# Optimization experiments

Measured on AMD Instinct MI355X. Metric: run time of the kernel, lower is better.

The kernel has to match this reference:

```python
import jax, jax.numpy as jnp
import numpy as np

ALPHAS = (0.1, 0.3, 0.6)
WEIGHTS = (0.5, 0.3, 0.2)
HUBER_MARGIN = 1.0
B, S = 2048, 8192


def setup_inputs() -> dict:
    key = jax.random.key(0)
    k1, k2 = jax.random.split(key)
    pred = jax.random.normal(k1, (B, S), dtype=jnp.float32)
    target = jax.random.normal(k2, (B, S), dtype=jnp.float32)
    return {"pred": pred, "target": target}


def _ema(x, alpha):
    # x: [B, S]; ema[0] = x[0]; ema[i] = alpha*x[i] + (1-alpha)*ema[i-1]
    x0 = x[:, 0]
    def step(carry, xi):
        nc = alpha * xi + (1.0 - alpha) * carry
        return nc, nc
    _, ys = jax.lax.scan(step, x0, x[:, 1:].T)  # ys: [S-1, B]
    return jnp.concatenate([x0[:, None], ys.T], axis=1)  # [B, S]


def _huber_loss(pred_delta, target_delta):
    dir_agreement = pred_delta * target_delta
    step_err = jnp.abs(pred_delta - target_delta)
    quad = jnp.square(jnp.maximum(HUBER_MARGIN - dir_agreement, 0.0)) / (2.0 * HUBER_MARGIN)
    return jnp.where(dir_agreement < 0, step_err, quad).mean(axis=1)  # [B]


def reference(pred, target):
    loss = jnp.zeros((pred.shape[0],), dtype=pred.dtype)
    for alpha, weight in zip(ALPHAS, WEIGHTS):
        pe = _ema(pred, alpha)
        te = _ema(target, alpha)
        pd = pe[:, 1:] - pe[:, :-1]
        td = te[:, 1:] - te[:, :-1]
        loss = loss + weight * _huber_loss(pd, td)
    return loss.mean()  # reduction='mean'
```

## Files before the change

### kernel.cpp

```cpp
#include <hip/hip_runtime.h>

#define B_ROWS 2048
#define S_LEN  8192
#define PER_LANE 16
#define TPB 512
#define WPB 8
#define CHUNK (64 * PER_LANE)
#define NBLOCKS B_ROWS

constexpr double cpowi(double b, int e) { double r = 1.0; for (int i = 0; i < e; ++i) r *= b; return r; }
constexpr float tof(double x) { return (x < 1.2e-38 && x > -1.2e-38) ? 0.0f : (float)x; }

#define W0f 0.9f
#define W1f 0.7f
#define W2f 0.4f
#define SE0 0.2f
#define SE1 0.6f
#define SE2 1.2f
constexpr float NA0 = -(0.1f * 0.1f);
constexpr float NA1 = -(0.3f * 0.3f);
constexpr float NA2 = -(0.6f * 0.6f);

constexpr float D0_1 = tof(cpowi(0.9, 16)),  D0_2 = tof(cpowi(0.9, 32));
constexpr float D0_4 = tof(cpowi(0.9, 64)),  D0_8 = tof(cpowi(0.9, 128));
constexpr float D1_1 = tof(cpowi(0.7, 16)),  D1_2 = tof(cpowi(0.7, 32));
constexpr float D2_1 = tof(cpowi(0.4, 16));

#define L2_0 (-0.15200309344504997f)
#define L2_1 (-0.51457317282975830f)
#define L2_2 (-1.32192809488736230f)

__device__ __forceinline__ float scan4(float v, int lane, float d1, float d2, float d4, float d8) {
    float u;
    u = __shfl_up(v, 1); v += (lane >= 1 ? d1 : 0.0f) * u;
    u = __shfl_up(v, 2); v += (lane >= 2 ? d2 : 0.0f) * u;
    u = __shfl_up(v, 4); v += (lane >= 4 ? d4 : 0.0f) * u;
    u = __shfl_up(v, 8); v += (lane >= 8 ? d8 : 0.0f) * u;
    return v;
}
__device__ __forceinline__ float scan2(float v, int lane, float d1, float d2) {
    float u;
    u = __shfl_up(v, 1); v += (lane >= 1 ? d1 : 0.0f) * u;
    u = __shfl_up(v, 2); v += (lane >= 2 ? d2 : 0.0f) * u;
    return v;
}
__device__ __forceinline__ float scan1(float v, int lane, float d1) {
    float u;
    u = __shfl_up(v, 1); v += (lane >= 1 ? d1 : 0.0f) * u;
    return v;
}

__global__ void __launch_bounds__(TPB, 4) msl_main(const float* __restrict__ pred,
                                                   const float* __restrict__ targ,
                                                   float* __restrict__ partial) {
    const int lane = threadIdx.x & 63;
    const int wave = threadIdx.x >> 6;
    const float* __restrict__ prow = pred + (size_t)blockIdx.x * S_LEN;
    const float* __restrict__ trow = targ + (size_t)blockIdx.x * S_LEN;
    const int base = wave * CHUNK + lane * PER_LANE;

    __shared__ float dxs[WPB][2][PER_LANE][64];
    __shared__ float sex[WPB][6];
    __shared__ float sred[WPB];

    const bool w0 = (wave == 0);
    const bool lz = (lane == 0);

    float pv0p = 0.f, pv0t = 0.f;
    if (lz && wave > 0) { pv0p = prow[base - 1]; pv0t = trow[base - 1]; }

    float xp[PER_LANE], xt[PER_LANE];
    {
        const float4* p4 = reinterpret_cast<const float4*>(prow + base);
        const float4* t4 = reinterpret_cast<const float4*>(trow + base);
#pragma unroll
        for (int j = 0; j < PER_LANE / 4; ++j) {
            float4 a = p4[j];
            float4 b = t4[j];
            xp[4 * j + 0] = a.x; xp[4 * j + 1] = a.y; xp[4 * j + 2] = a.z; xp[4 * j + 3] = a.w;
            xt[4 * j + 0] = b.x; xt[4 * j + 1] = b.y; xt[4 * j + 2] = b.z; xt[4 * j + 3] = b.w;
        }
    }

    float pvp = __shfl_up(xp[PER_LANE - 1], 1);
    float pvt = __shfl_up(xt[PER_LANE - 1], 1);
    if (lz) {
        pvp = w0 ? xp[0] : pv0p;
        pvt = w0 ? xt[0] : pv0t;
    }

    float Mp0 = 0.f, Mp1 = 0.f, Mp2 = 0.f, Mt0 = 0.f, Mt1 = 0.f, Mt2 = 0.f;
    float prevp = pvp, prevt = pvt;
#pragma unroll
    for (int j = 0; j < PER_LANE; ++j) {
        float dxp = xp[j] - prevp; prevp = xp[j];
        float dxt = xt[j] - prevt; prevt = xt[j];
        dxs[wave][0][j][lane] = dxp;
        dxs[wave][1][j][lane] = dxt;
        Mp0 = fmaf(W0f, Mp0, dxp);
        Mp1 = fmaf(W1f, Mp1, dxp);
        Mp2 = fmaf(W2f, Mp2, dxp);
        Mt0 = fmaf(W0f, Mt0, dxt);
        Mt1 = fmaf(W1f, Mt1, dxt);
        Mt2 = fmaf(W2f, Mt2, dxt);
    }

    float vp0 = scan4(Mp0, lane, D0_1, D0_2, D0_4, D0_8);
    float vp1 = scan2(Mp1, lane, D1_1, D1_2);
    float vp2 = scan1(Mp2, lane, D2_1);
    float vt0 = scan4(Mt0, lane, D0_1, D0_2, D0_4, D0_8);
    float vt1 = scan2(Mt1, lane, D1_1, D1_2);
    float vt2 = scan1(Mt2, lane, D2_1);

    if (lane == 63) {
        sex[wave][0] = vp0; sex[wave][1] = vp1; sex[wave][2] = vp2;
        sex[wave][3] = vt0; sex[wave][4] = vt1; sex[wave][5] = vt2;
    }
    __syncthreads();

    float Cp0 = 0.f, Cp1 = 0.f, Cp2 = 0.f, Ct0 = 0.f, Ct1 = 0.f, Ct2 = 0.f;
    if (wave > 0) {
        Cp0 = sex[wave - 1][0]; Cp1 = sex[wave - 1][1]; Cp2 = sex[wave - 1][2];
        Ct0 = sex[wave - 1][3]; Ct1 = sex[wave - 1][4]; Ct2 = sex[wave - 1][5];
    }

    const float e  = (float)(PER_LANE * lane);
    const float G0 = exp2f(e * L2_0);
    const float G1 = exp2f(e * L2_1);
    const float G2 = exp2f(e * L2_2);

    float up0 = __shfl_up(vp0, 1), up1 = __shfl_up(vp1, 1), up2 = __shfl_up(vp2, 1);
    float ut0 = __shfl_up(vt0, 1), ut1 = __shfl_up(vt1, 1), ut2 = __shfl_up(vt2, 1);

    float yp0 = lz ? (w0 ? 0.0f : Cp0) : fmaf(G0, Cp0, up0);
    float yp1 = lz ? (w0 ? 0.0f : Cp1) : fmaf(G1, Cp1, up1);
    float yp2 = lz ? (w0 ? 0.0f : Cp2) : fmaf(G2, Cp2, up2);
    float yt0 = lz ? (w0 ? 0.0f : Ct0) : fmaf(G0, Ct0, ut0);
    float yt1 = lz ? (w0 ? 0.0f : Ct1) : fmaf(G1, Ct1, ut1);
    float yt2 = lz ? (w0 ? 0.0f : Ct2) : fmaf(G2, Ct2, ut2);

    float acc0 = 0.f, acc1 = 0.f, acc2 = 0.f;
    const float skip = (w0 && lz) ? 0.0f : 1.0f;
#pragma unroll
    for (int j = 0; j < PER_LANE; ++j) {
        float dxp = dxs[wave][0][j][lane];
        float dxt = dxs[wave][1][j][lane];
        yp0 = fmaf(W0f, yp0, dxp);
        yt0 = fmaf(W0f, yt0, dxt);
        yp1 = fmaf(W1f, yp1, dxp);
        yt1 = fmaf(W1f, yt1, dxt);
        yp2 = fmaf(W2f, yp2, dxp);
        yt2 = fmaf(W2f, yt2, dxt);

        float m0 = yp0 * yt0, m1 = yp1 * yt1, m2 = yp2 * yt2;
        float se0 = SE0 * fabsf(yp0 - yt0);
        float se1 = SE1 * fabsf(yp1 - yt1);
        float se2 = SE2 * fabsf(yp2 - yt2);
        float mm0 = fmaxf(fmaf(NA0, m0, 1.0f), 0.0f);
        float mm1 = fmaxf(fmaf(NA1, m1, 1.0f), 0.0f);
        float mm2 = fmaxf(fmaf(NA2, m2, 1.0f), 0.0f);
        float h0 = (m0 < 0.0f) ? se0 : mm0 * mm0;
        float h1 = (m1 < 0.0f) ? se1 : mm1 * mm1;
        float h2 = (m2 < 0.0f) ? se2 : mm2 * mm2;
        if (j == 0) { h0 *= skip; h1 *= skip; h2 *= skip; }
        acc0 += h0; acc1 += h1; acc2 += h2;
    }

    float wacc = 0.25f * acc0 + 0.15f * acc1 + 0.10f * acc2;
#pragma unroll
    for (int o = 32; o > 0; o >>= 1) wacc += __shfl_down(wacc, o);

    if (lz) sred[wave] = wacc;
    __syncthreads();
    if (threadIdx.x == 0) {
        float s = 0.f;
#pragma unroll
        for (int i = 0; i < WPB; ++i) s += sred[i];
        partial[blockIdx.x] = s;
    }
}

__global__ void __launch_bounds__(256) msl_reduce(const float* __restrict__ partial,
                                                  float* __restrict__ out) {
    const int tid = threadIdx.x;
    float v = 0.f;
#pragma unroll
    for (int k = 0; k < NBLOCKS / 256; ++k) v += partial[tid + 256 * k];
#pragma unroll
    for (int o = 32; o > 0; o >>= 1) v += __shfl_down(v, o);
    __shared__ float s[4];
    if ((tid & 63) == 0) s[tid >> 6] = v;
    __syncthreads();
    if (tid == 0)
        out[0] = (s[0] + s[1] + s[2] + s[3]) *
                 (float)(1.0 / ((double)(S_LEN - 1) * (double)B_ROWS));
}

extern "C" void kernel_launch(void* const* d_in, const int* in_sizes, int n_in,
                              void* d_out, int out_size, void* d_ws, size_t ws_size,
                              hipStream_t stream) {
    const float* pred = (const float*)d_in[0];
    const float* targ = (const float*)d_in[1];
    float* out = (float*)d_out;
    float* partial = (float*)d_ws;

    msl_main<<<NBLOCKS, TPB, 0, stream>>>(pred, targ, partial);
    msl_reduce<<<1, 256, 0, stream>>>(partial, out);
}
```

Measured before the change: 143.9 us.

## Make wave chunks independent via halo-based EMA carry recomputation

Each wave now handles one 1024-element chunk of a row on its own. Instead of taking the previous chunk's EMA carry from another wave through shared memory and a block barrier, it recomputes an approximate carry from a 256-element halo before the chunk. Because the decay factors are below one, the truncated history adds negligible error. Blocks shrink to 4 waves with a higher occupancy hint, and one dx value stays in a register to trim shared memory. The cost is extra halo loads and extra shuffle scans per wave.

```diff
diff --git a/kernel.cpp b/kernel.cpp
--- a/kernel.cpp
+++ b/kernel.cpp
@@ -3,10 +3,13 @@
 #define B_ROWS 2048
 #define S_LEN  8192
 #define PER_LANE 16
-#define TPB 512
-#define WPB 8
 #define CHUNK (64 * PER_LANE)
-#define NBLOCKS B_ROWS
+#define CPR (S_LEN / CHUNK)
+#define TPB 256
+#define WPB 4
+#define NCHUNK (B_ROWS * CPR)
+#define NBLOCKS (NCHUNK / WPB)
+#define HALO 256
 
 constexpr double cpowi(double b, int e) { double r = 1.0; for (int i = 0; i < e; ++i) r *= b; return r; }
 constexpr float tof(double x) { return (x < 1.2e-38 && x > -1.2e-38) ? 0.0f : (float)x; }
@@ -25,11 +28,40 @@
 constexpr float D0_4 = tof(cpowi(0.9, 64)),  D0_8 = tof(cpowi(0.9, 128));
 constexpr float D1_1 = tof(cpowi(0.7, 16)),  D1_2 = tof(cpowi(0.7, 32));
 constexpr float D2_1 = tof(cpowi(0.4, 16));
+constexpr float H0_1 = tof(cpowi(0.9, 4)),   H0_2 = tof(cpowi(0.9, 8));
+constexpr float H0_4 = tof(cpowi(0.9, 16)),  H0_8 = tof(cpowi(0.9, 32));
+constexpr float H0_16 = tof(cpowi(0.9, 64)), H0_32 = tof(cpowi(0.9, 128));
+constexpr float H1_1 = tof(cpowi(0.7, 4)),   H1_2 = tof(cpowi(0.7, 8));
+constexpr float H1_4 = tof(cpowi(0.7, 16)),  H1_8 = tof(cpowi(0.7, 32));
+constexpr float H1_16 = tof(cpowi(0.7, 64));
+constexpr float H2_1 = tof(cpowi(0.4, 4)),   H2_2 = tof(cpowi(0.4, 8));
+constexpr float H2_4 = tof(cpowi(0.4, 16));
 
 #define L2_0 (-0.15200309344504997f)
 #define L2_1 (-0.51457317282975830f)
 #define L2_2 (-1.32192809488736230f)
 
+__device__ __forceinline__ float scan6(float v, int lane, float d1, float d2, float d4,
+                                       float d8, float d16, float d32) {
+    float u;
+    u = __shfl_up(v, 1);  v += (lane >= 1  ? d1  : 0.0f) * u;
+    u = __shfl_up(v, 2);  v += (lane >= 2  ? d2  : 0.0f) * u;
+    u = __shfl_up(v, 4);  v += (lane >= 4  ? d4  : 0.0f) * u;
+    u = __shfl_up(v, 8);  v += (lane >= 8  ? d8  : 0.0f) * u;
+    u = __shfl_up(v, 16); v += (lane >= 16 ? d16 : 0.0f) * u;
+    u = __shfl_up(v, 32); v += (lane >= 32 ? d32 : 0.0f) * u;
+    return v;
+}
+__device__ __forceinline__ float scan5(float v, int lane, float d1, float d2, float d4,
+                                       float d8, float d16) {
+    float u;
+    u = __shfl_up(v, 1);  v += (lane >= 1  ? d1  : 0.0f) * u;
+    u = __shfl_up(v, 2);  v += (lane >= 2  ? d2  : 0.0f) * u;
+    u = __shfl_up(v, 4);  v += (lane >= 4  ? d4  : 0.0f) * u;
+    u = __shfl_up(v, 8);  v += (lane >= 8  ? d8  : 0.0f) * u;
+    u = __shfl_up(v, 16); v += (lane >= 16 ? d16 : 0.0f) * u;
+    return v;
+}
 __device__ __forceinline__ float scan4(float v, int lane, float d1, float d2, float d4, float d8) {
     float u;
     u = __shfl_up(v, 1); v += (lane >= 1 ? d1 : 0.0f) * u;
@@ -38,6 +70,13 @@
     u = __shfl_up(v, 8); v += (lane >= 8 ? d8 : 0.0f) * u;
     return v;
 }
+__device__ __forceinline__ float scan3(float v, int lane, float d1, float d2, float d4) {
+    float u;
+    u = __shfl_up(v, 1); v += (lane >= 1 ? d1 : 0.0f) * u;
+    u = __shfl_up(v, 2); v += (lane >= 2 ? d2 : 0.0f) * u;
+    u = __shfl_up(v, 4); v += (lane >= 4 ? d4 : 0.0f) * u;
+    return v;
+}
 __device__ __forceinline__ float scan2(float v, int lane, float d1, float d2) {
     float u;
     u = __shfl_up(v, 1); v += (lane >= 1 ? d1 : 0.0f) * u;
@@ -50,24 +89,25 @@
     return v;
 }
 
-__global__ void __launch_bounds__(TPB, 4) msl_main(const float* __restrict__ pred,
+__global__ void __launch_bounds__(TPB, 5) msl_main(const float* __restrict__ pred,
                                                    const float* __restrict__ targ,
                                                    float* __restrict__ partial) {
     const int lane = threadIdx.x & 63;
     const int wave = threadIdx.x >> 6;
-    const float* __restrict__ prow = pred + (size_t)blockIdx.x * S_LEN;
-    const float* __restrict__ trow = targ + (size_t)blockIdx.x * S_LEN;
-    const int base = wave * CHUNK + lane * PER_LANE;
-
-    __shared__ float dxs[WPB][2][PER_LANE][64];
-    __shared__ float sex[WPB][6];
+    const int gcid = blockIdx.x * WPB + wave;
+    const int row  = gcid >> 3;
+    const int cid  = gcid & (CPR - 1);
+    const float* __restrict__ prow = pred + (size_t)row * S_LEN;
+    const float* __restrict__ trow = targ + (size_t)row * S_LEN;
+    const int co   = cid * CHUNK;
+    const int base = co + lane * PER_LANE;
+
+    __shared__ float dxs[WPB][2][PER_LANE - 1][64];
     __shared__ float sred[WPB];
 
-    const bool w0 = (wave == 0);
-    const bool lz = (lane == 0);
-
-    float pv0p = 0.f, pv0t = 0.f;
-    if (lz && wave > 0) { pv0p = prow[base - 1]; pv0t = trow[base - 1]; }
+    const bool lz     = (lane == 0);
+    const bool haloed = (cid != 0);
+    const bool head   = (!haloed) && lz;
 
     float xp[PER_LANE], xt[PER_LANE];
     {
@@ -82,21 +122,55 @@
         }
     }
 
+    float Cp0 = 0.f, Cp1 = 0.f, Cp2 = 0.f, Ct0 = 0.f, Ct1 = 0.f, Ct2 = 0.f;
+    float lastp = xp[0], lastt = xt[0];
+    if (haloed) {
+        float hp[4], ht[4];
+        {
+            float4 a = *reinterpret_cast<const float4*>(prow + co - HALO + lane * 4);
+            float4 b = *reinterpret_cast<const float4*>(trow + co - HALO + lane * 4);
+            hp[0] = a.x; hp[1] = a.y; hp[2] = a.z; hp[3] = a.w;
+            ht[0] = b.x; ht[1] = b.y; ht[2] = b.z; ht[3] = b.w;
+        }
+        float php = __shfl_up(hp[3], 1);
+        float pht = __shfl_up(ht[3], 1);
+        if (lz) { php = hp[0]; pht = ht[0]; }
+
+        float Ap0 = 0.f, Ap1 = 0.f, Ap2 = 0.f, At0 = 0.f, At1 = 0.f, At2 = 0.f;
+#pragma unroll
+        for (int s = 0; s < 4; ++s) {
+            float dxp = hp[s] - php; php = hp[s];
+            float dxt = ht[s] - pht; pht = ht[s];
+            Ap0 = fmaf(W0f, Ap0, dxp);
+            Ap1 = fmaf(W1f, Ap1, dxp);
+            Ap2 = fmaf(W2f, Ap2, dxp);
+            At0 = fmaf(W0f, At0, dxt);
+            At1 = fmaf(W1f, At1, dxt);
+            At2 = fmaf(W2f, At2, dxt);
+        }
+        float vh;
+        vh = scan6(Ap0, lane, H0_1, H0_2, H0_4, H0_8, H0_16, H0_32); Cp0 = __shfl(vh, 63);
+        vh = scan5(Ap1, lane, H1_1, H1_2, H1_4, H1_8, H1_16);        Cp1 = __shfl(vh, 63);
+        vh = scan3(Ap2, lane, H2_1, H2_2, H2_4);                     Cp2 = __shfl(vh, 63);
+        vh = scan6(At0, lane, H0_1, H0_2, H0_4, H0_8, H0_16, H0_32); Ct0 = __shfl(vh, 63);
+        vh = scan5(At1, lane, H1_1, H1_2, H1_4, H1_8, H1_16);        Ct1 = __shfl(vh, 63);
+        vh = scan3(At2, lane, H2_1, H2_2, H2_4);                     Ct2 = __shfl(vh, 63);
+        lastp = __shfl(hp[3], 63);
+        lastt = __shfl(ht[3], 63);
+    }
+
     float pvp = __shfl_up(xp[PER_LANE - 1], 1);
     float pvt = __shfl_up(xt[PER_LANE - 1], 1);
-    if (lz) {
-        pvp = w0 ? xp[0] : pv0p;
-        pvt = w0 ? xt[0] : pv0t;
-    }
-
+    if (lz) { pvp = lastp; pvt = lastt; }
+
+    float dx0p, dx0t;
     float Mp0 = 0.f, Mp1 = 0.f, Mp2 = 0.f, Mt0 = 0.f, Mt1 = 0.f, Mt2 = 0.f;
-    float prevp = pvp, prevt = pvt;
 #pragma unroll
     for (int j = 0; j < PER_LANE; ++j) {
-        float dxp = xp[j] - prevp; prevp = xp[j];
-        float dxt = xt[j] - prevt; prevt = xt[j];
-        dxs[wave][0][j][lane] = dxp;
-        dxs[wave][1][j][lane] = dxt;
+        float dxp = xp[j] - pvp; pvp = xp[j];
+        float dxt = xt[j] - pvt; pvt = xt[j];
+        if (j == 0) { dx0p = dxp; dx0t = dxt; }
+        else        { dxs[wave][0][j - 1][lane] = dxp; dxs[wave][1][j - 1][lane] = dxt; }
         Mp0 = fmaf(W0f, Mp0, dxp);
         Mp1 = fmaf(W1f, Mp1, dxp);
         Mp2 = fmaf(W2f, Mp2, dxp);
@@ -112,18 +186,6 @@
     float vt1 = scan2(Mt1, lane, D1_1, D1_2);
     float vt2 = scan1(Mt2, lane, D2_1);
 
-    if (lane == 63) {
-        sex[wave][0] = vp0; sex[wave][1] = vp1; sex[wave][2] = vp2;
-        sex[wave][3] = vt0; sex[wave][4] = vt1; sex[wave][5] = vt2;
-    }
-    __syncthreads();
-
-    float Cp0 = 0.f, Cp1 = 0.f, Cp2 = 0.f, Ct0 = 0.f, Ct1 = 0.f, Ct2 = 0.f;
-    if (wave > 0) {
-        Cp0 = sex[wave - 1][0]; Cp1 = sex[wave - 1][1]; Cp2 = sex[wave - 1][2];
-        Ct0 = sex[wave - 1][3]; Ct1 = sex[wave - 1][4]; Ct2 = sex[wave - 1][5];
-    }
-
     const float e  = (float)(PER_LANE * lane);
     const float G0 = exp2f(e * L2_0);
     const float G1 = exp2f(e * L2_1);
@@ -132,19 +194,19 @@
     float up0 = __shfl_up(vp0, 1), up1 = __shfl_up(vp1, 1), up2 = __shfl_up(vp2, 1);
     float ut0 = __shfl_up(vt0, 1), ut1 = __shfl_up(vt1, 1), ut2 = __shfl_up(vt2, 1);
 
-    float yp0 = lz ? (w0 ? 0.0f : Cp0) : fmaf(G0, Cp0, up0);
-    float yp1 = lz ? (w0 ? 0.0f : Cp1) : fmaf(G1, Cp1, up1);
-    float yp2 = lz ? (w0 ? 0.0f : Cp2) : fmaf(G2, Cp2, up2);
-    float yt0 = lz ? (w0 ? 0.0f : Ct0) : fmaf(G0, Ct0, ut0);
-    float yt1 = lz ? (w0 ? 0.0f : Ct1) : fmaf(G1, Ct1, ut1);
-    float yt2 = lz ? (w0 ? 0.0f : Ct2) : fmaf(G2, Ct2, ut2);
+    float yp0 = lz ? Cp0 : fmaf(G0, Cp0, up0);
+    float yp1 = lz ? Cp1 : fmaf(G1, Cp1, up1);
+    float yp2 = lz ? Cp2 : fmaf(G2, Cp2, up2);
+    float yt0 = lz ? Ct0 : fmaf(G0, Ct0, ut0);
+    float yt1 = lz ? Ct1 : fmaf(G1, Ct1, ut1);
+    float yt2 = lz ? Ct2 : fmaf(G2, Ct2, ut2);
 
     float acc0 = 0.f, acc1 = 0.f, acc2 = 0.f;
-    const float skip = (w0 && lz) ? 0.0f : 1.0f;
+    const float skip = head ? 0.0f : 1.0f;
 #pragma unroll
     for (int j = 0; j < PER_LANE; ++j) {
-        float dxp = dxs[wave][0][j][lane];
-        float dxt = dxs[wave][1][j][lane];
+        float dxp = (j == 0) ? dx0p : dxs[wave][0][j - 1][lane];
+        float dxt = (j == 0) ? dx0t : dxs[wave][1][j - 1][lane];
         yp0 = fmaf(W0f, yp0, dxp);
         yt0 = fmaf(W0f, yt0, dxt);
         yp1 = fmaf(W1f, yp1, dxp);
@@ -172,12 +234,8 @@
 
     if (lz) sred[wave] = wacc;
     __syncthreads();
-    if (threadIdx.x == 0) {
-        float s = 0.f;
-#pragma unroll
-        for (int i = 0; i < WPB; ++i) s += sred[i];
-        partial[blockIdx.x] = s;
-    }
+    if (threadIdx.x == 0)
+        partial[blockIdx.x] = sred[0] + sred[1] + sred[2] + sred[3];
 }
 
 __global__ void __launch_bounds__(256) msl_reduce(const float* __restrict__ partial,
```

Result: no change. 143.7 us (-0.2%).
